# Performance work log

Hardware: AMD Instinct MI355X
Metric: run time of the kernel (lower is better)

Reference implementation:

```python
import jax, jax.numpy as jnp
import numpy as np

B, D = 4096, 1024

def setup_inputs() -> dict:
    key = jax.random.key(0)
    k1, k2, k3 = jax.random.split(key, 3)
    # q, p are row-stochastic probability distributions (original calls q.log())
    q = jax.nn.softmax(jax.random.normal(k1, (B, D), dtype=jnp.float32), axis=-1)
    p = jax.nn.softmax(jax.random.normal(k2, (B, D), dtype=jnp.float32), axis=-1)
    # binary same-class indicator matrix
    labels_matrix = jax.random.randint(k3, (B, B), 0, 2).astype(jnp.float32)
    return {"q": q, "p": p, "labels_matrix": labels_matrix}

def reference(q, p, labels_matrix):
    d = q.shape[1]
    log_q = jnp.log(q)
    log_p = jnp.log(p)
    # torch kl_div(log_q, p) = p * (log p - log q); mean over feature dim -> [B]
    kl_div = jnp.mean(p * (log_p - log_q), axis=1)
    # pairwise kl_dis[i, j] = mean_d p[j,d] * (log p[j,d] - log q[i,d])
    # = (sum_d p[j] log p[j] - (log_q @ p^T)[i, j]) / D  -- single GEMM, no BxBxD tensor
    p_entropy_term = jnp.sum(p * log_p, axis=1)          # [B]
    cross = log_q @ p.T                                   # [B, B]
    kl_dis = (p_entropy_term[None, :] - cross) / d        # [B, B]
    # original detaches kl_dis via .cpu().numpy()
    kl_dis = jax.lax.stop_gradient(kl_dis)
    positive = kl_div + jnp.sum(kl_dis * labels_matrix, axis=1)
    negative = jnp.sum(kl_dis * (1.0 - labels_matrix), axis=1)
    return jnp.sum(positive / negative)
```

## Files before the change

kernel.cpp:

```cpp
#include <hip/hip_runtime.h>
#include <hip/hip_bf16.h>
#include <stdint.h>

#define BROWS 4096
#define DDIM  1024

typedef __bf16 bf16_t;
typedef __bf16 bf16x8 __attribute__((ext_vector_type(8)));
typedef float  f32x4  __attribute__((ext_vector_type(4)));

__device__ __forceinline__ unsigned short f2bf_bits(float f) {
    union { float f; unsigned int u; } v; v.f = f;
    unsigned int u = v.u;
    unsigned int r = (u + 0x7fffu + ((u >> 16) & 1u)) >> 16;
    return (unsigned short)r;
}

__global__ __launch_bounds__(256) void prep_kernel(
    const float* __restrict__ q, const float* __restrict__ p,
    const float* __restrict__ L,
    bf16_t* __restrict__ lqb, bf16_t* __restrict__ pb,
    uint64_t* __restrict__ Lb,
    float* __restrict__ e, float* __restrict__ kld,
    float* __restrict__ CS, float* __restrict__ CL, float* __restrict__ EL)
{
    const int row = blockIdx.x;
    const int t   = threadIdx.x;
    const int wv  = t >> 6, ln = t & 63;

    const float4* q4 = (const float4*)(q + (size_t)row * DDIM);
    const float4* p4 = (const float4*)(p + (size_t)row * DDIM);
    float4 qv = q4[t];
    float4 pv = p4[t];

    float lq0 = __logf(qv.x), lq1 = __logf(qv.y), lq2 = __logf(qv.z), lq3 = __logf(qv.w);
    float lp0 = __logf(pv.x), lp1 = __logf(pv.y), lp2 = __logf(pv.z), lp3 = __logf(pv.w);

    float esum = pv.x * lp0 + pv.y * lp1 + pv.z * lp2 + pv.w * lp3;
    float ksum = pv.x * (lp0 - lq0) + pv.y * (lp1 - lq1)
               + pv.z * (lp2 - lq2) + pv.w * (lp3 - lq3);

    ushort4 uq, up;
    uq.x = f2bf_bits(lq0); uq.y = f2bf_bits(lq1); uq.z = f2bf_bits(lq2); uq.w = f2bf_bits(lq3);
    up.x = f2bf_bits(pv.x); up.y = f2bf_bits(pv.y); up.z = f2bf_bits(pv.z); up.w = f2bf_bits(pv.w);
    ((ushort4*)(lqb + (size_t)row * DDIM))[t] = uq;
    ((ushort4*)(pb  + (size_t)row * DDIM))[t] = up;

    const float* Lrow = L + (size_t)row * BROWS;
    #pragma unroll
    for (int c = 0; c < 16; c++) {
        float v = Lrow[c * 256 + t];
        unsigned long long m = __ballot(v != 0.0f);
        if (ln == 0) Lb[(size_t)row * 64 + c * 4 + wv] = m;
    }

    if (t == 0) { CS[row] = 0.f; CL[row] = 0.f; EL[row] = 0.f; }

    #pragma unroll
    for (int off = 32; off > 0; off >>= 1) {
        esum += __shfl_down(esum, off);
        ksum += __shfl_down(ksum, off);
    }
    __shared__ float se[4], sk[4];
    if (ln == 0) { se[wv] = esum; sk[wv] = ksum; }
    __syncthreads();
    if (t == 0) {
        e[row]   = se[0] + se[1] + se[2] + se[3];
        kld[row] = (sk[0] + sk[1] + sk[2] + sk[3]) * (1.0f / DDIM);
    }
}

__global__ __launch_bounds__(64, 4) void gemm_epi_kernel(
    const bf16_t* __restrict__ Abf,
    const bf16_t* __restrict__ Bbf,
    const uint64_t* __restrict__ Lb,
    const float*  __restrict__ e,
    float* __restrict__ CS, float* __restrict__ CL, float* __restrict__ EL)
{
    __shared__ bf16_t As[64 * 32];
    __shared__ bf16_t Bs[64 * 32];

    const int lane = threadIdx.x;
    const int i0   = blockIdx.y * 64;
    const int j0   = blockIdx.x * 64;
    const int q4   = lane >> 4;
    const int ln   = lane & 15;

    f32x4 acc[4][4];
    #pragma unroll
    for (int a = 0; a < 4; a++)
        #pragma unroll
        for (int b = 0; b < 4; b++)
            acc[a][b] = (f32x4){0.f, 0.f, 0.f, 0.f};

    const bf16_t* gA[4];
    const bf16_t* gB[4];
    int ldsoff[4];
    #pragma unroll
    for (int n = 0; n < 4; n++) {
        const int c = n * 64 + lane;
        const int r = c >> 2;
        const int col = (c & 3) * 8;
        gA[n] = Abf + (size_t)(i0 + r) * DDIM + col;
        gB[n] = Bbf + (size_t)(j0 + r) * DDIM + col;
        ldsoff[n] = c * 8;
    }

    #pragma unroll 1
    for (int k0 = 0; k0 < DDIM; k0 += 32) {
        #pragma unroll
        for (int n = 0; n < 4; n++)
            __builtin_amdgcn_global_load_lds(
                (const __attribute__((address_space(1))) void*)(gA[n] + k0),
                (__attribute__((address_space(3))) void*)(As + ldsoff[n]), 16, 0, 0);
        #pragma unroll
        for (int n = 0; n < 4; n++)
            __builtin_amdgcn_global_load_lds(
                (const __attribute__((address_space(1))) void*)(gB[n] + k0),
                (__attribute__((address_space(3))) void*)(Bs + ldsoff[n]), 16, 0, 0);

        bf16x8 af[4], bfr[4];
        #pragma unroll
        for (int mi = 0; mi < 4; mi++)
            af[mi] = *(const bf16x8*)(As + (mi * 16 + ln) * 32 + q4 * 8);
        #pragma unroll
        for (int ni = 0; ni < 4; ni++)
            bfr[ni] = *(const bf16x8*)(Bs + (ni * 16 + ln) * 32 + q4 * 8);
        #pragma unroll
        for (int mi = 0; mi < 4; mi++)
            #pragma unroll
            for (int ni = 0; ni < 4; ni++)
                acc[mi][ni] = __builtin_amdgcn_mfma_f32_16x16x32_bf16(
                    af[mi], bfr[ni], acc[mi][ni], 0, 0, 0);
    }

    float e_j[4];
    #pragma unroll
    for (int ni = 0; ni < 4; ni++) e_j[ni] = e[j0 + ni * 16 + ln];

    #pragma unroll
    for (int mi = 0; mi < 4; mi++) {
        #pragma unroll
        for (int r = 0; r < 4; r++) {
            const int i = i0 + mi * 16 + q4 * 4 + r;
            const uint64_t m  = Lb[(size_t)i * 64 + (j0 >> 6)];
            const uint64_t ms = m >> ln;
            float cs = 0.f, cl = 0.f, el = 0.f;
            #pragma unroll
            for (int ni = 0; ni < 4; ni++) {
                float c = acc[mi][ni][r];
                cs += c;
                if ((ms >> (ni * 16)) & 1ull) { cl += c; el += e_j[ni]; }
            }
            #pragma unroll
            for (int s = 1; s < 16; s <<= 1) {
                cs += __shfl_xor(cs, s);
                cl += __shfl_xor(cl, s);
                el += __shfl_xor(el, s);
            }
            if (ln == 0) {
                atomicAdd(&CS[i], cs);
                atomicAdd(&CL[i], cl);
                atomicAdd(&EL[i], el);
            }
        }
    }
}

__global__ __launch_bounds__(256) void final_kernel(
    const float* __restrict__ e, const float* __restrict__ kld,
    const float* __restrict__ CS, const float* __restrict__ CL,
    const float* __restrict__ EL, float* __restrict__ out)
{
    __shared__ float sred[4];
    __shared__ float sEtot;
    const int t = threadIdx.x;

    float s = 0.f;
    for (int j = t; j < BROWS; j += 256) s += e[j];
    #pragma unroll
    for (int off = 32; off > 0; off >>= 1) s += __shfl_down(s, off);
    if ((t & 63) == 0) sred[t >> 6] = s;
    __syncthreads();
    if (t == 0) sEtot = sred[0] + sred[1] + sred[2] + sred[3];
    __syncthreads();
    const float Etot = sEtot;
    const float invD = 1.0f / DDIM;

    float rs = 0.f;
    for (int i = t; i < BROWS; i += 256) {
        float el = EL[i], cl = CL[i], cs = CS[i];
        float pos = kld[i] + (el - cl) * invD;
        float neg = (Etot - el - cs + cl) * invD;
        rs += pos / neg;
    }
    __syncthreads();
    #pragma unroll
    for (int off = 32; off > 0; off >>= 1) rs += __shfl_down(rs, off);
    if ((t & 63) == 0) sred[t >> 6] = rs;
    __syncthreads();
    if (t == 0) out[0] = sred[0] + sred[1] + sred[2] + sred[3];
}

extern "C" void kernel_launch(void* const* d_in, const int* in_sizes, int n_in,
                              void* d_out, int out_size, void* d_ws, size_t ws_size,
                              hipStream_t stream)
{
    const float* q = (const float*)d_in[0];
    const float* p = (const float*)d_in[1];
    const float* L = (const float*)d_in[2];
    float* out = (float*)d_out;

    char* ws = (char*)d_ws;
    bf16_t* lqb = (bf16_t*)ws;
    bf16_t* pb  = (bf16_t*)(ws + (size_t)BROWS * DDIM * 2);
    float*  e   = (float*)(ws + (size_t)BROWS * DDIM * 4);
    float*  kld = e + BROWS;
    float*  CS  = kld + BROWS;
    float*  CL  = CS + BROWS;
    float*  EL  = CL + BROWS;
    uint64_t* Lb = (uint64_t*)(EL + BROWS);

    prep_kernel<<<BROWS, 256, 0, stream>>>(q, p, L, lqb, pb, Lb, e, kld, CS, CL, EL);

    dim3 grid(BROWS / 64, BROWS / 64);
    gemm_epi_kernel<<<grid, 64, 0, stream>>>(lqb, pb, Lb, e, CS, CL, EL);

    final_kernel<<<1, 256, 0, stream>>>(e, kld, CS, CL, EL, out);
}
```

Before: 214.8 us.

## Enlarge GEMM block tile to 256x128 with 8 waves and register-prefetched LDS staging

Replaces the single-wave 64x64 GEMM block with a 512-thread block computing a 256x128 tile. Each wave keeps its 64x64 sub-tile. Operands are staged through padded LDS in K chunks of 64, and the next chunk is prefetched into registers while the current one is consumed, with barriers guarding the buffer. This raises operand reuse per global load and overlaps loads with MFMA work, at the cost of more LDS per block and two barriers per chunk.

```diff
diff --git a/kernel.cpp b/kernel.cpp
--- a/kernel.cpp
+++ b/kernel.cpp
@@ -8,6 +8,8 @@
 typedef __bf16 bf16_t;
 typedef __bf16 bf16x8 __attribute__((ext_vector_type(8)));
 typedef float  f32x4  __attribute__((ext_vector_type(4)));
+
+#define LDS_STRIDE 68
 
 __device__ __forceinline__ unsigned short f2bf_bits(float f) {
     union { float f; unsigned int u; } v; v.f = f;
@@ -70,21 +72,25 @@
     }
 }
 
-__global__ __launch_bounds__(64, 4) void gemm_epi_kernel(
+__global__ __launch_bounds__(512, 4) void gemm_epi_kernel(
     const bf16_t* __restrict__ Abf,
     const bf16_t* __restrict__ Bbf,
     const uint64_t* __restrict__ Lb,
     const float*  __restrict__ e,
     float* __restrict__ CS, float* __restrict__ CL, float* __restrict__ EL)
 {
-    __shared__ bf16_t As[64 * 32];
-    __shared__ bf16_t Bs[64 * 32];
-
-    const int lane = threadIdx.x;
-    const int i0   = blockIdx.y * 64;
-    const int j0   = blockIdx.x * 64;
+    __shared__ __align__(16) bf16_t As[256 * LDS_STRIDE];
+    __shared__ __align__(16) bf16_t Bs[128 * LDS_STRIDE];
+
+    const int t    = threadIdx.x;
+    const int i0   = blockIdx.y * 256;
+    const int j0   = blockIdx.x * 128;
+    const int wave = t >> 6;
+    const int lane = t & 63;
     const int q4   = lane >> 4;
     const int ln   = lane & 15;
+    const int wrow = wave & 3;
+    const int wcol = wave >> 2;
 
     f32x4 acc[4][4];
     #pragma unroll
@@ -93,57 +99,77 @@
         for (int b = 0; b < 4; b++)
             acc[a][b] = (f32x4){0.f, 0.f, 0.f, 0.f};
 
-    const bf16_t* gA[4];
-    const bf16_t* gB[4];
-    int ldsoff[4];
+    const bf16_t* gAp[4]; int lA[4];
+    const bf16_t* gBp[2]; int lB[2];
     #pragma unroll
     for (int n = 0; n < 4; n++) {
-        const int c = n * 64 + lane;
-        const int r = c >> 2;
-        const int col = (c & 3) * 8;
-        gA[n] = Abf + (size_t)(i0 + r) * DDIM + col;
-        gB[n] = Bbf + (size_t)(j0 + r) * DDIM + col;
-        ldsoff[n] = c * 8;
-    }
+        const int id = t + n * 512;
+        gAp[n] = Abf + (size_t)(i0 + (id >> 3)) * DDIM + (id & 7) * 8;
+        lA[n]  = (id >> 3) * LDS_STRIDE + (id & 7) * 8;
+    }
+    #pragma unroll
+    for (int n = 0; n < 2; n++) {
+        const int id = t + n * 512;
+        gBp[n] = Bbf + (size_t)(j0 + (id >> 3)) * DDIM + (id & 7) * 8;
+        lB[n]  = (id >> 3) * LDS_STRIDE + (id & 7) * 8;
+    }
+
+    bf16x8 pfA[4], pfB[2];
+    #pragma unroll
+    for (int n = 0; n < 4; n++) pfA[n] = *(const bf16x8*)(gAp[n]);
+    #pragma unroll
+    for (int n = 0; n < 2; n++) pfB[n] = *(const bf16x8*)(gBp[n]);
 
     #pragma unroll 1
-    for (int k0 = 0; k0 < DDIM; k0 += 32) {
-        #pragma unroll
-        for (int n = 0; n < 4; n++)
-            __builtin_amdgcn_global_load_lds(
-                (const __attribute__((address_space(1))) void*)(gA[n] + k0),
-                (__attribute__((address_space(3))) void*)(As + ldsoff[n]), 16, 0, 0);
-        #pragma unroll
-        for (int n = 0; n < 4; n++)
-            __builtin_amdgcn_global_load_lds(
-                (const __attribute__((address_space(1))) void*)(gB[n] + k0),
-                (__attribute__((address_space(3))) void*)(Bs + ldsoff[n]), 16, 0, 0);
-
-        bf16x8 af[4], bfr[4];
-        #pragma unroll
-        for (int mi = 0; mi < 4; mi++)
-            af[mi] = *(const bf16x8*)(As + (mi * 16 + ln) * 32 + q4 * 8);
-        #pragma unroll
-        for (int ni = 0; ni < 4; ni++)
-            bfr[ni] = *(const bf16x8*)(Bs + (ni * 16 + ln) * 32 + q4 * 8);
-        #pragma unroll
-        for (int mi = 0; mi < 4; mi++)
+    for (int c = 0; c < DDIM / 64; ++c) {
+        __syncthreads();
+        #pragma unroll
+        for (int n = 0; n < 4; n++) *(bf16x8*)(As + lA[n]) = pfA[n];
+        #pragma unroll
+        for (int n = 0; n < 2; n++) *(bf16x8*)(Bs + lB[n]) = pfB[n];
+        __syncthreads();
+
+        if (c < DDIM / 64 - 1) {
+            const int k = (c + 1) * 64;
+            #pragma unroll
+            for (int n = 0; n < 4; n++) pfA[n] = *(const bf16x8*)(gAp[n] + k);
+            #pragma unroll
+            for (int n = 0; n < 2; n++) pfB[n] = *(const bf16x8*)(gBp[n] + k);
+        }
+
+        #pragma unroll
+        for (int ks = 0; ks < 2; ks++) {
+            bf16x8 af[4], bfr[4];
+            #pragma unroll
+            for (int mi = 0; mi < 4; mi++)
+                af[mi] = *(const bf16x8*)(As + (wrow * 64 + mi * 16 + ln) * LDS_STRIDE
+                                             + ks * 32 + q4 * 8);
             #pragma unroll
             for (int ni = 0; ni < 4; ni++)
-                acc[mi][ni] = __builtin_amdgcn_mfma_f32_16x16x32_bf16(
-                    af[mi], bfr[ni], acc[mi][ni], 0, 0, 0);
-    }
+                bfr[ni] = *(const bf16x8*)(Bs + (wcol * 64 + ni * 16 + ln) * LDS_STRIDE
+                                              + ks * 32 + q4 * 8);
+            #pragma unroll
+            for (int mi = 0; mi < 4; mi++)
+                #pragma unroll
+                for (int ni = 0; ni < 4; ni++)
+                    acc[mi][ni] = __builtin_amdgcn_mfma_f32_16x16x32_bf16(
+                        af[mi], bfr[ni], acc[mi][ni], 0, 0, 0);
+        }
+    }
+
+    const int i_base = i0 + wrow * 64;
+    const int j_base = j0 + wcol * 64;
 
     float e_j[4];
     #pragma unroll
-    for (int ni = 0; ni < 4; ni++) e_j[ni] = e[j0 + ni * 16 + ln];
+    for (int ni = 0; ni < 4; ni++) e_j[ni] = e[j_base + ni * 16 + ln];
 
     #pragma unroll
     for (int mi = 0; mi < 4; mi++) {
         #pragma unroll
         for (int r = 0; r < 4; r++) {
-            const int i = i0 + mi * 16 + q4 * 4 + r;
-            const uint64_t m  = Lb[(size_t)i * 64 + (j0 >> 6)];
+            const int i = i_base + mi * 16 + q4 * 4 + r;
+            const uint64_t m  = Lb[(size_t)i * 64 + (j_base >> 6)];
             const uint64_t ms = m >> ln;
             float cs = 0.f, cl = 0.f, el = 0.f;
             #pragma unroll
@@ -223,8 +249,8 @@
 
     prep_kernel<<<BROWS, 256, 0, stream>>>(q, p, L, lqb, pb, Lb, e, kld, CS, CL, EL);
 
-    dim3 grid(BROWS / 64, BROWS / 64);
-    gemm_epi_kernel<<<grid, 64, 0, stream>>>(lqb, pb, Lb, e, CS, CL, EL);
+    dim3 grid(BROWS / 128, BROWS / 256);
+    gemm_epi_kernel<<<grid, 512, 0, stream>>>(lqb, pb, Lb, e, CS, CL, EL);
 
     final_kernel<<<1, 256, 0, stream>>>(e, kld, CS, CL, EL, out);
 }
```

Result: faster. 190.4 us (-11.4%).
